# Kernel tuning notes

Measured on AMD Instinct MI355X. Metric: run time of the kernel, lower is better.

The kernel has to match this reference:

```python
import jax, jax.numpy as jnp
import numpy as np

HEADS = 8
DIM_HEAD = 64
SCALE = DIM_HEAD ** -0.5


def setup_inputs() -> dict:
    key = jax.random.key(0)
    k1, k2, k3 = jax.random.split(key, 3)
    b, p, n, dim = 2, 16, 512, 512
    inner = HEADS * DIM_HEAD  # 512
    x = jax.random.normal(k1, (b, p, n, dim), dtype=jnp.float32)
    W_qkv = jax.random.normal(k2, (dim, 3 * inner), dtype=jnp.float32) * (dim ** -0.5)
    W_out = jax.random.normal(k3, (inner, dim), dtype=jnp.float32) * (inner ** -0.5)
    b_out = jnp.zeros((dim,), dtype=jnp.float32)
    return {"x": x, "W_qkv": W_qkv, "W_out": W_out, "b_out": b_out}


def reference(x, W_qkv, W_out, b_out):
    b, p, n, dim = x.shape
    # QKV projection (no bias), split into q, k, v
    qkv = jnp.einsum('bpnd,de->bpne', x, W_qkv)
    q, k, v = jnp.split(qkv, 3, axis=-1)
    # (b, p, n, h*d) -> (b, p, h, n, d)
    def to_heads(t):
        return t.reshape(b, p, n, HEADS, DIM_HEAD).transpose(0, 1, 3, 2, 4)
    q, k, v = to_heads(q), to_heads(k), to_heads(v)
    # attention scores: (b, p, h, n, n)
    dots = jnp.einsum('bphnd,bphmd->bphnm', q, k) * SCALE
    attn = jax.nn.softmax(dots, axis=-1)
    out = jnp.einsum('bphnm,bphmd->bphnd', attn, v)
    # (b, p, h, n, d) -> (b, p, n, h*d)
    out = out.transpose(0, 1, 3, 2, 4).reshape(b, p, n, HEADS * DIM_HEAD)
    # output projection (dropout rate = 0.0 -> identity)
    return jnp.einsum('bpne,ed->bpnd', out, W_out) + b_out
```

## Files before the change

### kernel.cpp

```cpp
#include <hip/hip_runtime.h>
#include <hip/hip_bf16.h>

typedef short bf16x8 __attribute__((ext_vector_type(8)));
typedef short bf16x4 __attribute__((ext_vector_type(4)));
typedef float f32x4  __attribute__((ext_vector_type(4)));

__device__ __forceinline__ unsigned short f2bf(float f) {
    union { float fv; unsigned int u; } v; v.fv = f;
    unsigned int r = v.u + 0x7FFFu + ((v.u >> 16) & 1u);
    return (unsigned short)(r >> 16);
}

__device__ __forceinline__ short f2bf_n(float f) {
    union { __hip_bfloat16 h; short s; } u;
    u.h = __float2bfloat16(f);
    return u.s;
}

__device__ __forceinline__ void gload16(const short* g, short* l) {
    __builtin_amdgcn_global_load_lds(
        (const __attribute__((address_space(1))) void*)g,
        (__attribute__((address_space(3))) void*)l, 16, 0, 0);
}

__global__ __launch_bounds__(256) void prep_all(
    const float* __restrict__ x, short* __restrict__ xb,
    const float* __restrict__ Wqkv, const float* __restrict__ Wout,
    short* __restrict__ Wqkvt, short* __restrict__ Woutt)
{
    if (blockIdx.x < 4096) {
        size_t i = ((size_t)blockIdx.x * 256 + threadIdx.x) * 8;
        f32x4 a = *(const f32x4*)(x + i);
        f32x4 b = *(const f32x4*)(x + i + 4);
        bf16x8 s;
        #pragma unroll
        for (int e = 0; e < 4; ++e) { s[e] = (short)f2bf(a[e]); s[4 + e] = (short)f2bf(b[e]); }
        *(bf16x8*)(xb + i) = s;
        return;
    }
    __shared__ float tile[32][33];
    const int b = blockIdx.x - 4096;
    const float* src; short* dst; int N, bb;
    if (b < 768) { src = Wqkv; dst = Wqkvt; N = 1536; bb = b; }
    else         { src = Wout; dst = Woutt; N = 512;  bb = b - 768; }
    const int tx = threadIdx.x;
    const int nb = N >> 5;
    const int k0 = (bb / nb) * 32;
    const int n0 = (bb % nb) * 32;
    const int r  = tx >> 3;
    const int c4 = (tx & 7) * 4;
    f32x4 v = *(const f32x4*)(src + (size_t)(k0 + r) * N + n0 + c4);
    #pragma unroll
    for (int e = 0; e < 4; ++e) tile[r][c4 + e] = v[e];
    __syncthreads();
    bf16x4 o;
    #pragma unroll
    for (int e = 0; e < 4; ++e) o[e] = (short)f2bf(tile[c4 + e][r]);
    *(bf16x4*)(dst + (size_t)(n0 + r) * 512 + k0 + c4) = o;
}

template<int F32OUT>
__global__ __launch_bounds__(256, 2) void gemm_db(
    const short* __restrict__ A, const short* __restrict__ Bt,
    short* __restrict__ Cb, float* __restrict__ Cf, const float* __restrict__ bias,
    int M, int N, int K, int NB)
{
    __shared__ short lds[2][2][128 * 64];
    const int t    = threadIdx.x;
    const int lane = t & 63;
    const int wid  = t >> 6;
    const int l15  = lane & 15;
    const int lg   = lane >> 4;

    const int cpx = gridDim.x >> 3;
    const int swz = (blockIdx.x & 7) * cpx + (blockIdx.x >> 3);
    const int m0 = (swz / NB) * 128;
    const int n0 = (swz % NB) * 128;

    const int wm = (wid >> 1) * 64;
    const int wn = (wid & 1) * 64;

    const int scol = 8 * ((lane & 7) ^ ((lane >> 3) & 7));

    float bval[4];
    if constexpr (F32OUT) {
        #pragma unroll
        for (int ni = 0; ni < 4; ++ni) bval[ni] = bias[n0 + wn + ni * 16 + l15];
    }

    f32x4 acc[4][4];
    #pragma unroll
    for (int i = 0; i < 4; ++i)
        #pragma unroll
        for (int j = 0; j < 4; ++j)
            acc[i][j] = f32x4{0.f, 0.f, 0.f, 0.f};

    const int NT = K >> 6;

    auto stage = [&](int buf, int tk) {
        #pragma unroll
        for (int j = 0; j < 4; ++j) {
            const int r = wid * 32 + j * 8 + (lane >> 3);
            gload16(A  + (size_t)(m0 + r) * K + tk * 64 + scol,
                    &lds[buf][0][(wid * 32 + j * 8) * 64]);
            gload16(Bt + (size_t)(n0 + r) * K + tk * 64 + scol,
                    &lds[buf][1][(wid * 32 + j * 8) * 64]);
        }
    };

    stage(0, 0);

    for (int tk = 0; tk < NT; ++tk) {
        const int cur = tk & 1;
        if (tk + 1 < NT) {
            stage(cur ^ 1, tk + 1);
            asm volatile("s_waitcnt vmcnt(8)" ::: "memory");
        } else {
            asm volatile("s_waitcnt vmcnt(0)" ::: "memory");
        }
        __builtin_amdgcn_s_barrier();

        bf16x8 af[4][2], bg[4][2];
        #pragma unroll
        for (int kk = 0; kk < 2; ++kk) {
            #pragma unroll
            for (int mi = 0; mi < 4; ++mi)
                af[mi][kk] = *(const bf16x8*)&lds[cur][0][
                    (wm + mi * 16 + l15) * 64 + (((kk * 4 + lg) ^ (l15 & 7)) * 8)];
            #pragma unroll
            for (int ni = 0; ni < 4; ++ni)
                bg[ni][kk] = *(const bf16x8*)&lds[cur][1][
                    (wn + ni * 16 + l15) * 64 + (((kk * 4 + lg) ^ (l15 & 7)) * 8)];
        }

        __builtin_amdgcn_s_setprio(1);
        #pragma unroll
        for (int kk = 0; kk < 2; ++kk)
            #pragma unroll
            for (int mi = 0; mi < 4; ++mi)
                #pragma unroll
                for (int ni = 0; ni < 4; ++ni)
                    acc[mi][ni] = __builtin_amdgcn_mfma_f32_16x16x32_bf16(
                        af[mi][kk], bg[ni][kk], acc[mi][ni], 0, 0, 0);
        __builtin_amdgcn_s_setprio(0);
        __builtin_amdgcn_s_barrier();
    }

    #pragma unroll
    for (int mi = 0; mi < 4; ++mi) {
        #pragma unroll
        for (int ni = 0; ni < 4; ++ni) {
            const int col = n0 + wn + ni * 16 + l15;
            #pragma unroll
            for (int r = 0; r < 4; ++r) {
                const int rowi = m0 + wm + mi * 16 + 4 * lg + r;
                if constexpr (F32OUT) {
                    Cf[(size_t)rowi * N + col] = acc[mi][ni][r] + bval[ni];
                } else {
                    Cb[(size_t)rowi * N + col] = (short)f2bf(acc[mi][ni][r]);
                }
            }
        }
    }
}

__global__ __launch_bounds__(512, 4) void attn_kernel(
    const short* __restrict__ qkv, short* __restrict__ attn_out)
{
    __shared__ short Kl[2][4096];
    __shared__ short Vt[2][5120];
    const int t    = threadIdx.x;
    const int lane = t & 63;
    const int wid  = t >> 6;
    const int l15  = lane & 15;
    const int lg   = lane >> 4;
    const int pairid = blockIdx.x & 255;
    const int qh  = blockIdx.x >> 8;
    const int bp  = pairid >> 3;
    const int h   = pairid & 7;
    const size_t tok0 = (size_t)bp * 512;
    const int q0   = qh * 256 + wid * 32;
    const int qcol = h * 64;

    bf16x8 qf[2][2];
    #pragma unroll
    for (int mj = 0; mj < 2; ++mj)
        #pragma unroll
        for (int kf = 0; kf < 2; ++kf)
            qf[mj][kf] = *(const bf16x8*)(qkv + (tok0 + q0 + mj * 16 + l15) * 1536
                                          + qcol + kf * 32 + 8 * lg);

    f32x4 ot[4][2];
    #pragma unroll
    for (int i = 0; i < 4; ++i)
        #pragma unroll
        for (int j = 0; j < 2; ++j)
            ot[i][j] = f32x4{0.f, 0.f, 0.f, 0.f};
    float mrun[2] = {-1e30f, -1e30f}, lrun[2] = {0.f, 0.f};

    const int krow = t >> 3;
    const short* Ksrc0 = qkv + (tok0 + krow) * 1536 + 512 + qcol
                         + 8 * ((t & 7) ^ (krow & 7));
    const int sn = t >> 3;
    const int sd = (t & 7) * 8;
    const short* Vsrc0 = qkv + (tok0 + sn) * 1536 + 1024 + qcol + sd;
    const int kvp = (sn & 7) | (((sn >> 3) ^ (t & 7)) << 3);

    gload16(Ksrc0, &Kl[0][t * 8]);
    bf16x8 vreg = *(const bf16x8*)(Vsrc0);

    const float C = 0.18033688011112042f;

    for (int tkv = 0; tkv < 8; ++tkv) {
        const int cur = tkv & 1;
        #pragma unroll
        for (int i = 0; i < 8; ++i)
            Vt[cur][(sd + i) * 80 + kvp] = vreg[i];
        __syncthreads();
        if (tkv < 7) {
            gload16(Ksrc0 + (size_t)(tkv + 1) * 64 * 1536, &Kl[cur ^ 1][t * 8]);
            vreg = *(const bf16x8*)(Vsrc0 + (size_t)(tkv + 1) * 64 * 1536);
        }

        f32x4 st[4][2];
        #pragma unroll
        for (int i = 0; i < 4; ++i)
            #pragma unroll
            for (int j = 0; j < 2; ++j)
                st[i][j] = f32x4{0.f, 0.f, 0.f, 0.f};
        __builtin_amdgcn_s_setprio(1);
        #pragma unroll
        for (int kf = 0; kf < 2; ++kf) {
            #pragma unroll
            for (int ni = 0; ni < 4; ++ni) {
                bf16x8 kfr = *(const bf16x8*)&Kl[cur][
                    (ni * 16 + l15) * 64 + (((kf * 4 + lg) ^ (l15 & 7)) * 8)];
                #pragma unroll
                for (int mj = 0; mj < 2; ++mj)
                    st[ni][mj] = __builtin_amdgcn_mfma_f32_16x16x32_bf16(
                        kfr, qf[mj][kf], st[ni][mj], 0, 0, 0);
            }
        }
        __builtin_amdgcn_s_setprio(0);

        #pragma unroll
        for (int mj = 0; mj < 2; ++mj) {
            float pm = -1e30f;
            #pragma unroll
            for (int ni = 0; ni < 4; ++ni)
                #pragma unroll
                for (int r = 0; r < 4; ++r)
                    pm = fmaxf(pm, st[ni][mj][r]);
            pm = fmaxf(pm, __shfl_xor(pm, 16));
            pm = fmaxf(pm, __shfl_xor(pm, 32));
            pm *= C;
            if (!__all(pm <= mrun[mj] + 8.f)) {
                const float mnew = fmaxf(mrun[mj], pm);
                const float fsc  = __builtin_amdgcn_exp2f(mrun[mj] - mnew);
                lrun[mj] *= fsc;
                #pragma unroll
                for (int di = 0; di < 4; ++di) ot[di][mj] *= fsc;
                mrun[mj] = mnew;
            }
            float ps = 0.f;
            #pragma unroll
            for (int ni = 0; ni < 4; ++ni)
                #pragma unroll
                for (int r = 0; r < 4; ++r) {
                    float e = __builtin_amdgcn_exp2f(
                        __builtin_fmaf(st[ni][mj][r], C, -mrun[mj]));
                    st[ni][mj][r] = e;
                    ps += e;
                }
            ps += __shfl_xor(ps, 16);
            ps += __shfl_xor(ps, 32);
            lrun[mj] += ps;
        }

        __builtin_amdgcn_s_setprio(1);
        #pragma unroll
        for (int ni = 0; ni < 4; ++ni) {
            bf16x4 pb[2];
            #pragma unroll
            for (int mj = 0; mj < 2; ++mj)
                #pragma unroll
                for (int r = 0; r < 4; ++r)
                    pb[mj][r] = f2bf_n(st[ni][mj][r]);
            #pragma unroll
            for (int di = 0; di < 4; ++di) {
                const int row = di * 16 + l15;
                bf16x4 av = *(const bf16x4*)&Vt[cur][
                    row * 80
                    + (((2 * ni + (lg >> 1)) ^ (2 * di + (l15 >> 3))) * 8)
                    + 4 * (lg & 1)];
                #pragma unroll
                for (int mj = 0; mj < 2; ++mj)
                    ot[di][mj] = __builtin_amdgcn_mfma_f32_16x16x16bf16_1k(
                        av, pb[mj], ot[di][mj], 0, 0, 0);
            }
        }
        __builtin_amdgcn_s_setprio(0);
    }

    float inv[2];
    #pragma unroll
    for (int mj = 0; mj < 2; ++mj) inv[mj] = 1.f / lrun[mj];
    #pragma unroll
    for (int di = 0; di < 4; ++di)
        #pragma unroll
        for (int mj = 0; mj < 2; ++mj) {
            const size_t tok = tok0 + q0 + mj * 16 + l15;
            const int col = qcol + di * 16 + 4 * lg;
            bf16x4 o4;
            #pragma unroll
            for (int r = 0; r < 4; ++r)
                o4[r] = f2bf_n(ot[di][mj][r] * inv[mj]);
            *(bf16x4*)(attn_out + tok * 512 + col) = o4;
        }
}

extern "C" void kernel_launch(void* const* d_in, const int* in_sizes, int n_in,
                              void* d_out, int out_size, void* d_ws, size_t ws_size,
                              hipStream_t stream) {
    const float* x    = (const float*)d_in[0];
    const float* Wqkv = (const float*)d_in[1];
    const float* Wout = (const float*)d_in[2];
    const float* bout = (const float*)d_in[3];
    float* out = (float*)d_out;

    char* ws = (char*)d_ws;
    short* qkvb  = (short*)(ws);
    short* xb    = (short*)(ws + 50331648ull);
    short* attnb = xb;
    short* Wqkvt = (short*)(ws + 67108864ull);
    short* Woutt = (short*)(ws + 68681728ull);

    prep_all<<<5120, 256, 0, stream>>>(x, xb, Wqkv, Wout, Wqkvt, Woutt);

    gemm_db<0><<<1536, 256, 0, stream>>>(xb, Wqkvt, qkvb, nullptr, nullptr,
                                         16384, 1536, 512, 12);

    attn_kernel<<<512, 512, 0, stream>>>(qkvb, attnb);

    gemm_db<1><<<512, 256, 0, stream>>>(attnb, Woutt, nullptr, out, bout,
                                        16384, 512, 512, 4);
}
```

Before: 96.14 us.

## Switch attention kernel to 32x32x16 MFMA tiles with in-register P relayout

Rewrites the attention inner loop to use 32x32x16 bf16 MFMA instructions for both QK^T and PV instead of 16x16 variants, so each wave holds one 32-row query tile with a single running max/sum. The softmax probabilities are packed with v_cvt_pk_bf16_f32 and redistributed across half-waves with v_permlane32_swap, feeding PV directly from registers. This cuts the instruction count, shuffle reductions and scalar bf16 conversions per tile. It relies on specific layout and swizzle index math matching the LDS layouts, and it changes register pressure.

```diff
diff --git a/kernel.cpp b/kernel.cpp
--- a/kernel.cpp
+++ b/kernel.cpp
@@ -4,6 +4,7 @@
 typedef short bf16x8 __attribute__((ext_vector_type(8)));
 typedef short bf16x4 __attribute__((ext_vector_type(4)));
 typedef float f32x4  __attribute__((ext_vector_type(4)));
+typedef float f32x16 __attribute__((ext_vector_type(16)));
 
 __device__ __forceinline__ unsigned short f2bf(float f) {
     union { float fv; unsigned int u; } v; v.fv = f;
@@ -15,6 +16,12 @@
     union { __hip_bfloat16 h; short s; } u;
     u.h = __float2bfloat16(f);
     return u.s;
+}
+
+__device__ __forceinline__ unsigned int cvtpk(float lo, float hi) {
+    unsigned int r;
+    asm volatile("v_cvt_pk_bf16_f32 %0, %1, %2" : "=v"(r) : "v"(lo), "v"(hi));
+    return r;
 }
 
 __device__ __forceinline__ void gload16(const short* g, short* l) {
@@ -172,8 +179,8 @@
     const int t    = threadIdx.x;
     const int lane = t & 63;
     const int wid  = t >> 6;
-    const int l15  = lane & 15;
-    const int lg   = lane >> 4;
+    const int l31  = lane & 31;
+    const int hi   = lane >> 5;
     const int pairid = blockIdx.x & 255;
     const int qh  = blockIdx.x >> 8;
     const int bp  = pairid >> 3;
@@ -182,21 +189,16 @@
     const int q0   = qh * 256 + wid * 32;
     const int qcol = h * 64;
 
-    bf16x8 qf[2][2];
-    #pragma unroll
-    for (int mj = 0; mj < 2; ++mj)
-        #pragma unroll
-        for (int kf = 0; kf < 2; ++kf)
-            qf[mj][kf] = *(const bf16x8*)(qkv + (tok0 + q0 + mj * 16 + l15) * 1536
-                                          + qcol + kf * 32 + 8 * lg);
-
-    f32x4 ot[4][2];
-    #pragma unroll
-    for (int i = 0; i < 4; ++i)
-        #pragma unroll
-        for (int j = 0; j < 2; ++j)
-            ot[i][j] = f32x4{0.f, 0.f, 0.f, 0.f};
-    float mrun[2] = {-1e30f, -1e30f}, lrun[2] = {0.f, 0.f};
+    bf16x8 qf[4];
+    #pragma unroll
+    for (int kf = 0; kf < 4; ++kf)
+        qf[kf] = *(const bf16x8*)(qkv + (tok0 + q0 + l31) * 1536
+                                  + qcol + kf * 16 + 8 * hi);
+
+    f32x16 ot0, ot1;
+    #pragma unroll
+    for (int r = 0; r < 16; ++r) { ot0[r] = 0.f; ot1[r] = 0.f; }
+    float mrun = -1e30f, lrun = 0.f;
 
     const int krow = t >> 3;
     const short* Ksrc0 = qkv + (tok0 + krow) * 1536 + 512 + qcol
@@ -222,101 +224,97 @@
             vreg = *(const bf16x8*)(Vsrc0 + (size_t)(tkv + 1) * 64 * 1536);
         }
 
-        f32x4 st[4][2];
-        #pragma unroll
-        for (int i = 0; i < 4; ++i)
-            #pragma unroll
-            for (int j = 0; j < 2; ++j)
-                st[i][j] = f32x4{0.f, 0.f, 0.f, 0.f};
+        f32x16 st0, st1;
+        #pragma unroll
+        for (int r = 0; r < 16; ++r) { st0[r] = 0.f; st1[r] = 0.f; }
         __builtin_amdgcn_s_setprio(1);
         #pragma unroll
-        for (int kf = 0; kf < 2; ++kf) {
-            #pragma unroll
-            for (int ni = 0; ni < 4; ++ni) {
-                bf16x8 kfr = *(const bf16x8*)&Kl[cur][
-                    (ni * 16 + l15) * 64 + (((kf * 4 + lg) ^ (l15 & 7)) * 8)];
-                #pragma unroll
-                for (int mj = 0; mj < 2; ++mj)
-                    st[ni][mj] = __builtin_amdgcn_mfma_f32_16x16x32_bf16(
-                        kfr, qf[mj][kf], st[ni][mj], 0, 0, 0);
-            }
+        for (int kf = 0; kf < 4; ++kf) {
+            const int slot = ((2 * kf + hi) ^ (l31 & 7)) * 8;
+            bf16x8 k0 = *(const bf16x8*)&Kl[cur][l31 * 64 + slot];
+            bf16x8 k1 = *(const bf16x8*)&Kl[cur][(32 + l31) * 64 + slot];
+            st0 = __builtin_amdgcn_mfma_f32_32x32x16_bf16(k0, qf[kf], st0, 0, 0, 0);
+            st1 = __builtin_amdgcn_mfma_f32_32x32x16_bf16(k1, qf[kf], st1, 0, 0, 0);
         }
         __builtin_amdgcn_s_setprio(0);
 
-        #pragma unroll
-        for (int mj = 0; mj < 2; ++mj) {
-            float pm = -1e30f;
-            #pragma unroll
-            for (int ni = 0; ni < 4; ++ni)
-                #pragma unroll
-                for (int r = 0; r < 4; ++r)
-                    pm = fmaxf(pm, st[ni][mj][r]);
-            pm = fmaxf(pm, __shfl_xor(pm, 16));
-            pm = fmaxf(pm, __shfl_xor(pm, 32));
-            pm *= C;
-            if (!__all(pm <= mrun[mj] + 8.f)) {
-                const float mnew = fmaxf(mrun[mj], pm);
-                const float fsc  = __builtin_amdgcn_exp2f(mrun[mj] - mnew);
-                lrun[mj] *= fsc;
-                #pragma unroll
-                for (int di = 0; di < 4; ++di) ot[di][mj] *= fsc;
-                mrun[mj] = mnew;
-            }
-            float ps = 0.f;
-            #pragma unroll
-            for (int ni = 0; ni < 4; ++ni)
-                #pragma unroll
-                for (int r = 0; r < 4; ++r) {
-                    float e = __builtin_amdgcn_exp2f(
-                        __builtin_fmaf(st[ni][mj][r], C, -mrun[mj]));
-                    st[ni][mj][r] = e;
-                    ps += e;
-                }
-            ps += __shfl_xor(ps, 16);
-            ps += __shfl_xor(ps, 32);
-            lrun[mj] += ps;
-        }
+        float pm = st0[0];
+        #pragma unroll
+        for (int r = 1; r < 16; ++r) pm = fmaxf(pm, st0[r]);
+        #pragma unroll
+        for (int r = 0; r < 16; ++r) pm = fmaxf(pm, st1[r]);
+        pm = fmaxf(pm, __shfl_xor(pm, 32));
+        pm *= C;
+        if (!__all(pm <= mrun + 8.f)) {
+            const float mnew = fmaxf(mrun, pm);
+            const float fsc  = __builtin_amdgcn_exp2f(mrun - mnew);
+            lrun *= fsc;
+            #pragma unroll
+            for (int r = 0; r < 16; ++r) { ot0[r] *= fsc; ot1[r] *= fsc; }
+            mrun = mnew;
+        }
+        float ps = 0.f;
+        #pragma unroll
+        for (int r = 0; r < 16; ++r) {
+            st0[r] = __builtin_amdgcn_exp2f(__builtin_fmaf(st0[r], C, -mrun));
+            ps += st0[r];
+        }
+        #pragma unroll
+        for (int r = 0; r < 16; ++r) {
+            st1[r] = __builtin_amdgcn_exp2f(__builtin_fmaf(st1[r], C, -mrun));
+            ps += st1[r];
+        }
+        ps += __shfl_xor(ps, 32);
+        lrun += ps;
 
         __builtin_amdgcn_s_setprio(1);
-        #pragma unroll
-        for (int ni = 0; ni < 4; ++ni) {
-            bf16x4 pb[2];
-            #pragma unroll
-            for (int mj = 0; mj < 2; ++mj)
-                #pragma unroll
-                for (int r = 0; r < 4; ++r)
-                    pb[mj][r] = f2bf_n(st[ni][mj][r]);
-            #pragma unroll
-            for (int di = 0; di < 4; ++di) {
-                const int row = di * 16 + l15;
-                bf16x4 av = *(const bf16x4*)&Vt[cur][
-                    row * 80
-                    + (((2 * ni + (lg >> 1)) ^ (2 * di + (l15 >> 3))) * 8)
-                    + 4 * (lg & 1)];
-                #pragma unroll
-                for (int mj = 0; mj < 2; ++mj)
-                    ot[di][mj] = __builtin_amdgcn_mfma_f32_16x16x16bf16_1k(
-                        av, pb[mj], ot[di][mj], 0, 0, 0);
-            }
-        }
+#define PVKS(KS, ST)                                                          \
+        {                                                                     \
+            const int a8 = ((KS) & 1) * 8;                                    \
+            unsigned int s0a = cvtpk(ST[a8 + 0], ST[a8 + 1]);                 \
+            unsigned int s0b = cvtpk(ST[a8 + 2], ST[a8 + 3]);                 \
+            unsigned int s1a = cvtpk(ST[a8 + 4], ST[a8 + 5]);                 \
+            unsigned int s1b = cvtpk(ST[a8 + 6], ST[a8 + 7]);                 \
+            asm volatile("v_permlane32_swap_b32 %0, %1"                       \
+                         : "+v"(s0a), "+v"(s1a));                             \
+            asm volatile("v_permlane32_swap_b32 %0, %1"                       \
+                         : "+v"(s0b), "+v"(s1b));                             \
+            union { unsigned int w[4]; bf16x8 v; } pu;                        \
+            pu.w[0] = s0a; pu.w[1] = s0b; pu.w[2] = s1a; pu.w[3] = s1b;       \
+            {                                                                 \
+                const int sl0 = ((2 * (KS) + hi) ^ (l31 >> 3)) * 8;           \
+                bf16x8 vf = *(const bf16x8*)&Vt[cur][l31 * 80 + sl0];         \
+                ot0 = __builtin_amdgcn_mfma_f32_32x32x16_bf16(                \
+                    vf, pu.v, ot0, 0, 0, 0);                                  \
+            }                                                                 \
+            {                                                                 \
+                const int sl1 = ((2 * (KS) + hi) ^ (4 ^ (l31 >> 3))) * 8;     \
+                bf16x8 vf = *(const bf16x8*)&Vt[cur][(32 + l31) * 80 + sl1];  \
+                ot1 = __builtin_amdgcn_mfma_f32_32x32x16_bf16(                \
+                    vf, pu.v, ot1, 0, 0, 0);                                  \
+            }                                                                 \
+        }
+        PVKS(0, st0)
+        PVKS(1, st0)
+        PVKS(2, st1)
+        PVKS(3, st1)
+#undef PVKS
         __builtin_amdgcn_s_setprio(0);
     }
 
-    float inv[2];
-    #pragma unroll
-    for (int mj = 0; mj < 2; ++mj) inv[mj] = 1.f / lrun[mj];
-    #pragma unroll
-    for (int di = 0; di < 4; ++di)
-        #pragma unroll
-        for (int mj = 0; mj < 2; ++mj) {
-            const size_t tok = tok0 + q0 + mj * 16 + l15;
-            const int col = qcol + di * 16 + 4 * lg;
-            bf16x4 o4;
-            #pragma unroll
-            for (int r = 0; r < 4; ++r)
-                o4[r] = f2bf_n(ot[di][mj][r] * inv[mj]);
-            *(bf16x4*)(attn_out + tok * 512 + col) = o4;
-        }
+    const float inv = 1.f / lrun;
+    short* obase = attn_out + (tok0 + q0 + l31) * 512 + qcol + 4 * hi;
+    #pragma unroll
+    for (int rq = 0; rq < 4; ++rq) {
+        bf16x4 o0, o1;
+        #pragma unroll
+        for (int j = 0; j < 4; ++j) {
+            o0[j] = f2bf_n(ot0[4 * rq + j] * inv);
+            o1[j] = f2bf_n(ot1[4 * rq + j] * inv);
+        }
+        *(bf16x4*)(obase + rq * 8)      = o0;
+        *(bf16x4*)(obase + 32 + rq * 8) = o1;
+    }
 }
 
 extern "C" void kernel_launch(void* const* d_in, const int* in_sizes, int n_in,
```

Measured after the change: 91.80 us, median of 3. 1.05x faster.
